# Kernel tuning notes

Measured on AMD Instinct MI355X. Metric: run time of the kernel, lower is better.

The kernel has to match this reference:

```python
import jax, jax.numpy as jnp
import numpy as np

N, M_X, M_G = 4096, 500, 50  # users, rating items, genre items


def setup_inputs() -> dict:
    key = jax.random.key(0)
    k1, k2, k3 = jax.random.split(key, 3)
    x_idx = jax.random.randint(k1, (N, M_X), 0, 6)          # ratings 0..5 (0 = pad)
    genre_idx = jax.random.randint(k2, (N, M_G), 0, 21)     # genre ids 0..20 (0 = pad)
    x1, x2, x3, x4, x5 = 3.0, 1.0, -1.0, -3.0, -5.0
    W_x = jnp.array([[0., 0., 0., 0., 0.],
                     [x1, x2, x3, x4, x5],
                     [x2, x1, x2, x3, x4],
                     [x3, x2, x1, x2, x3],
                     [x4, x3, x2, x1, x2],
                     [x5, x4, x3, x2, x1]], dtype=jnp.float32)  # [6,5]
    ohe_x = jnp.concatenate([jnp.zeros((1, 5)), jnp.eye(5)], axis=0).astype(jnp.float32)      # [6,5]
    W_genre = jax.random.normal(k3, (21, 20), dtype=jnp.float32)                              # [21,20]
    ohe_genre = jnp.concatenate([jnp.zeros((1, 20)), jnp.eye(20)], axis=0).astype(jnp.float32)  # [21,20]
    beta = jnp.array([1.0], dtype=jnp.float32)
    gamma = jnp.array([0.565], dtype=jnp.float32)
    coef = jnp.array([0.5, 0.001, 0.001], dtype=jnp.float32)
    return {"x_idx": x_idx, "genre_idx": genre_idx, "W_x": W_x, "ohe_x": ohe_x,
            "W_genre": W_genre, "ohe_genre": ohe_genre, "beta": beta, "gamma": gamma, "coef": coef}


def reference(x_idx, genre_idx, W_x, ohe_x, W_genre, ohe_genre, beta, gamma, coef):
    n = x_idx.shape[0]
    # Embeddings: table-lookup then flatten [N, items*dim]
    emb_x = W_x[x_idx].reshape(n, -1)        # [N, 2500]
    emb_xb = ohe_x[x_idx].reshape(n, -1)
    emb_g = W_genre[genre_idx].reshape(n, -1)  # [N, 1000]
    emb_gb = ohe_genre[genre_idx].reshape(n, -1)
    onehot = jnp.concatenate([emb_x, emb_g], axis=-1)       # [N, D]
    onehot_b = jnp.concatenate([emb_xb, emb_gb], axis=-1)   # [N, D]

    x = x_idx.astype(jnp.float32)            # [N, M]
    maskf = (x > 0).astype(jnp.float32)

    # Attention: one-hot similarity, diagonal mask, pow-temperature softmax
    sims = onehot @ onehot_b.T               # [N, N]
    sims = sims * (1.0 - jnp.eye(n, dtype=sims.dtype))
    temperature = jnp.power(jnp.max(sims, axis=1) + 0.001, gamma[0]) * beta[0]
    sim = jax.nn.softmax(sims / temperature[:, None], axis=1)

    mult = sim @ x                           # [N, M]
    scale = sim @ maskf + 0.0001             # [N, M]
    res = mult / scale

    # MeanAdd correction terms
    means_rows = x.sum(axis=1) / (maskf.sum(axis=1) + 1e-05)   # [N]
    means_cols = x.sum(axis=0) / (maskf.sum(axis=0) + 1e-05)   # [M]
    means_rows_m = maskf * means_rows[:, None]                 # [N, M]
    means_rows_sum = (sim @ means_rows_m) / scale
    means_rows_add = means_rows[:, None] - means_rows_sum
    add = (means_rows_add * coef[0]
           + (means_cols - means_cols.mean())[None, :] * coef[1]
           + (means_rows - means_rows.mean())[:, None] * coef[2])

    return jnp.clip(res + add, 1.0, 5.0)     # Hardtanh(1, 5)
```

## Files before the change

kernel.cpp:

```cpp
#include <hip/hip_runtime.h>
#include <hip/hip_bf16.h>
#include <stdint.h>

typedef unsigned short u16;
typedef unsigned int   u32;
typedef unsigned char  u8;
typedef long long      i64;
typedef __attribute__((ext_vector_type(8)))  __bf16 bf16x8;
typedef __attribute__((ext_vector_type(4)))  int    i32x4;
typedef __attribute__((ext_vector_type(16))) int    i32x16;
typedef __attribute__((ext_vector_type(16))) float  f32x16;

#define DEV __device__ __forceinline__

#define N_USERS 4096
#define MX      500
#define MG      50
#define K8      3584
#define RN      1536

#define OFF_A8  ((size_t)0)
#define OFF_B8  ((size_t)16777216)
#define OFF_P   ((size_t)0)
#define OFF_R   ((size_t)37748736)
#define OFF_S   ((size_t)58720256)
#define OFF_O   ((size_t)58720256)
#define OFF_SC  ((size_t)138412032)
#define OFF_WX8 (OFF_SC + 2048)
#define OFF_WG8 (OFF_SC + 2112)
#define OFF_MR  (OFF_SC + 4096)
#define OFF_MC  (OFF_SC + 4096 + 16384)
#define WS_REQUIRED (OFF_MC + 4096)

DEV u16 f2bf(float f) {
  union { float f; u32 u; } v; v.f = f;
  u32 r = v.u + 0x7FFFu + ((v.u >> 16) & 1u);
  return (u16)(r >> 16);
}
DEV float bf2f(u16 u) {
  union { u32 u; float f; } v; v.u = ((u32)u) << 16;
  return v.f;
}

DEV u8 f2fp8(float x) {
  union { float f; u32 u; } v; v.f = x;
  u32 s = (v.u >> 24) & 0x80u;
  float a = fabsf(x);
  if (a > 448.f) a = 448.f;
  if (a < 0.015625f) {
    int q = (int)rintf(a * 512.f);
    return (u8)(s | (u32)q);
  }
  v.f = a;
  int e = ((v.u >> 23) & 0xFF) - 127;
  u32 m = v.u & 0x7FFFFF;
  u32 mm = m >> 20;
  u32 rem = m & 0xFFFFF;
  if (rem > 0x80000u || (rem == 0x80000u && (mm & 1))) mm++;
  u32 out = (((u32)(e + 7)) << 3) + mm;
  if (out > 0x7Eu) out = 0x7Eu;
  return (u8)(s | out);
}

DEV void glds16(const void* g, void* l) {
  __builtin_amdgcn_global_load_lds(
      (const __attribute__((address_space(1))) void*)g,
      (__attribute__((address_space(3))) void*)l, 16, 0, 0);
}

__global__ __launch_bounds__(256) void k_prep(const void* wx, const void* wg,
                                              const void* beta, const void* gamma,
                                              const void* coef, float* sc,
                                              char* wx8, char* wg8) {
  __shared__ int sflag;
  int t = threadIdx.x;
  if (t == 0) {
    u32 u = ((const u32*)wx)[5];
    int f = (u == 0x40400000u) ? 1 : 0;
    sflag = f;
    ((int*)sc)[0] = f;
  }
  __syncthreads();
  int f = sflag;
  auto rd = [&](const void* p, int i) -> float {
    return f ? ((const float*)p)[i] : bf2f(((const u16*)p)[i]);
  };
  if (t == 0) {
    sc[1] = rd(beta, 0); sc[2] = rd(gamma, 0);
    sc[3] = rd(coef, 0); sc[4] = rd(coef, 1); sc[5] = rd(coef, 2);
  }
  for (int i = t; i < 30;  i += 256) wx8[i] = (char)__float2int_rn(rd(wx, i));
  for (int i = t; i < 420; i += 256) {
    int q = __float2int_rn(32.0f * rd(wg, i));
    q = (q > 127) ? 127 : ((q < -127) ? -127 : q);
    wg8[i] = (char)q;
  }
}

__global__ __launch_bounds__(64) void k_means_rows(const int* __restrict__ x, float* __restrict__ mr) {
  int i = blockIdx.x, t = threadIdx.x;
  const int* row = x + (size_t)i * MX;
  float s = 0.f, c = 0.f;
  for (int m = t; m < MX; m += 64) { int a = row[m]; s += (float)a; c += (a > 0) ? 1.f : 0.f; }
  for (int off = 32; off >= 1; off >>= 1) { s += __shfl_xor(s, off); c += __shfl_xor(c, off); }
  if (t == 0) mr[i] = s / (c + 1e-5f);
}

__global__ __launch_bounds__(256) void k_means_cols(const int* __restrict__ x, float* __restrict__ mc) {
  int m = blockIdx.x, t = threadIdx.x;
  float s = 0.f, c = 0.f;
  for (int i = t; i < N_USERS; i += 256) { int a = x[(size_t)i * MX + m]; s += (float)a; c += (a > 0) ? 1.f : 0.f; }
  __shared__ float ss[4], cs[4];
  for (int off = 32; off >= 1; off >>= 1) { s += __shfl_xor(s, off); c += __shfl_xor(c, off); }
  int w = t >> 6, lane = t & 63;
  if (lane == 0) { ss[w] = s; cs[w] = c; }
  __syncthreads();
  if (t == 0) {
    s = ss[0] + ss[1] + ss[2] + ss[3];
    c = cs[0] + cs[1] + cs[2] + cs[3];
    mc[m] = s / (c + 1e-5f);
  }
}

__global__ __launch_bounds__(256) void k_scalars(const float* __restrict__ mr, const float* __restrict__ mc, float* sc) {
  int t = threadIdx.x;
  float s1 = 0.f, s2 = 0.f;
  for (int i = t; i < N_USERS; i += 256) s1 += mr[i];
  for (int i = t; i < MX; i += 256) s2 += mc[i];
  __shared__ float a1[4], a2[4];
  for (int off = 32; off >= 1; off >>= 1) { s1 += __shfl_xor(s1, off); s2 += __shfl_xor(s2, off); }
  int w = t >> 6, lane = t & 63;
  if (lane == 0) { a1[w] = s1; a2[w] = s2; }
  __syncthreads();
  if (t == 0) {
    sc[6] = (a1[0] + a1[1] + a1[2] + a1[3]) / (float)N_USERS;
    sc[7] = (a2[0] + a2[1] + a2[2] + a2[3]) / (float)MX;
  }
}

__global__ __launch_bounds__(256) void k_buildAB(const int* __restrict__ xi, const int* __restrict__ gi,
                                                 const char* __restrict__ wx8, const char* __restrict__ wg8,
                                                 char* __restrict__ A8, char* __restrict__ B8) {
  int i = blockIdx.x, t = threadIdx.x;
  char* a8 = A8 + (size_t)i * K8;
  char* b8 = B8 + (size_t)i * K8;
  const int* xr = xi + (size_t)i * MX;
  const int* gr = gi + (size_t)i * MG;
  for (int m = t; m < MX; m += 256) {
    int a = xr[m];
    int base = m * 5;
#pragma unroll
    for (int d = 0; d < 5; ++d) {
      a8[base + d] = wx8[a * 5 + d];
      b8[base + d] = (a == d + 1) ? (char)32 : (char)0;
    }
  }
  for (int e = 2500 + t; e < 2560; e += 256) { a8[e] = 0; b8[e] = 0; }
  for (int m = t; m < MG; m += 256) {
    int g = gr[m];
    int base = 2560 + m * 20;
#pragma unroll
    for (int d = 0; d < 20; ++d) {
      a8[base + d] = wg8[g * 20 + d];
      b8[base + d] = (g == d + 1) ? (char)1 : (char)0;
    }
  }
  for (int e = 3560 + t; e < K8; e += 256) { a8[e] = 0; b8[e] = 0; }
}

__global__ __launch_bounds__(1024, 4) void k_gemm1(
    const char* __restrict__ A8, const char* __restrict__ B8,
    float* __restrict__ Cg, int N, int nt, int ld)
{
  extern __shared__ __align__(16) char ldsc[];
  int t = threadIdx.x, lane = t & 63, w = t >> 6;

  int nwg = gridDim.x * gridDim.y;
  int o = blockIdx.y * gridDim.x + blockIdx.x;
  int swz = (o & 7) * (nwg >> 3) + (o >> 3);
  int bn = swz % gridDim.x, bm = swz / gridDim.x;

  const char* pAb = A8 + (size_t)bm * 256 * ld;
  const char* pBb = B8 + (size_t)bn * 256 * ld;

  int wm = w >> 2, wn = w & 3;

  int aoffs[2][2], boffs[2][2];
#pragma unroll
  for (int m = 0; m < 2; ++m)
#pragma unroll
    for (int ks = 0; ks < 2; ++ks) {
      int row = wm * 64 + m * 32 + (lane & 31);
      int slot = ((ks << 1) | (lane >> 5)) ^ ((row & 3) ^ ((row >> 2) & 1));
      aoffs[m][ks] = row * 64 + slot * 16;
    }
#pragma unroll
  for (int n = 0; n < 2; ++n)
#pragma unroll
    for (int ks = 0; ks < 2; ++ks) {
      int col = wn * 64 + n * 32 + (lane & 31);
      int slot = ((ks << 1) | (lane >> 5)) ^ ((col & 3) ^ ((col >> 2) & 1));
      boffs[n][ks] = col * 64 + slot * 16;
    }

  const char* srcs[2]; int dsto[2];
  {
    const char* bp = (w < 8) ? pAb : pBb;
#pragma unroll
    for (int c = 0; c < 2; ++c) {
      int q = (w & 7) * 2 + c;
      int row = q * 16 + (lane >> 2);
      int slot = (lane & 3) ^ ((row & 3) ^ ((row >> 2) & 1));
      dsto[c] = ((w < 8) ? 0 : 16384) + q * 1024;
      srcs[c] = bp + (size_t)row * ld + slot * 16;
    }
  }

  auto stage = [&](int s) {
    if (s >= nt) return;
    char* dst = ldsc + ((size_t)(s & 3) << 15);
    size_t ko = (size_t)s * 64;
    glds16(srcs[0] + ko, dst + dsto[0]);
    glds16(srcs[1] + ko, dst + dsto[1]);
  };

#define STEP_TAIL(s)                                                        \
  do {                                                                      \
    int r_ = nt - 1 - (s);                                                  \
    if (r_ >= 3)      asm volatile("s_waitcnt vmcnt(4)" ::: "memory");      \
    else if (r_ == 2) asm volatile("s_waitcnt vmcnt(2)" ::: "memory");      \
    else if (r_ == 1) asm volatile("s_waitcnt vmcnt(0)" ::: "memory");      \
    if (r_ >= 1) {                                                          \
      __builtin_amdgcn_s_barrier();                                         \
      __builtin_amdgcn_sched_barrier(0);                                    \
    }                                                                       \
  } while (0)

  stage(0); stage(1); stage(2);
  asm volatile("s_waitcnt vmcnt(4)" ::: "memory");
  __builtin_amdgcn_s_barrier();
  __builtin_amdgcn_sched_barrier(0);

  i32x16 acc[2][2] = {};

  for (int s = 0; s < nt; ++s) {
    const char* At = ldsc + ((size_t)(s & 3) << 15);
    const char* Bt = At + 16384;
    stage(s + 3);
    i32x4 av[2][2], bv[2][2];
#pragma unroll
    for (int m = 0; m < 2; ++m)
#pragma unroll
      for (int ks = 0; ks < 2; ++ks) av[m][ks] = *(const i32x4*)(At + aoffs[m][ks]);
#pragma unroll
    for (int n = 0; n < 2; ++n)
#pragma unroll
      for (int ks = 0; ks < 2; ++ks) bv[n][ks] = *(const i32x4*)(Bt + boffs[n][ks]);
    __builtin_amdgcn_s_setprio(1);
#pragma unroll
    for (int ks = 0; ks < 2; ++ks)
#pragma unroll
      for (int m = 0; m < 2; ++m)
#pragma unroll
        for (int n = 0; n < 2; ++n)
          acc[m][n] = __builtin_amdgcn_mfma_i32_32x32x32_i8(av[m][ks], bv[n][ks], acc[m][n], 0, 0, 0);
    __builtin_amdgcn_s_setprio(0);
    STEP_TAIL(s);
  }
#undef STEP_TAIL

  int colb = bn * 256 + wn * 64 + (lane & 31);
  int rowb = bm * 256 + wm * 64 + ((lane >> 5) << 2);
#pragma unroll
  for (int m = 0; m < 2; ++m)
#pragma unroll
    for (int n = 0; n < 2; ++n) {
      float* Cp = Cg + (size_t)(rowb + m * 32) * N + colb + n * 32;
#pragma unroll
      for (int r = 0; r < 16; ++r) {
        int rr = (r & 3) + 8 * (r >> 2);
        Cp[(size_t)rr * N] = (float)acc[m][n][r] * 0.03125f;
      }
    }
}

__global__ __launch_bounds__(256, 2) void k_gemm2(
    const u8* __restrict__ Pg, const u8* __restrict__ Rg,
    float* __restrict__ Cg, int N, int nt, int ldp, int ldr)
{
  extern __shared__ __align__(16) char ldsc[];
  int t = threadIdx.x, lane = t & 63, w = t >> 6;

  int nwg = gridDim.x * gridDim.y;
  int o = blockIdx.y * gridDim.x + blockIdx.x;
  int swz = (o & 7) * (nwg >> 3) + (o >> 3);
  int bn = swz % gridDim.x, bm = swz / gridDim.x;

  const u8* pA = Pg + (size_t)bm * 128 * ldp;
  const u8* pB = Rg + (size_t)bn * 128 * ldr;

  int wm = w >> 1, wn = w & 1;

  int aoffs[2][4], boffs[2][4];
#pragma unroll
  for (int m = 0; m < 2; ++m)
#pragma unroll
    for (int kc = 0; kc < 4; ++kc) {
      int row = wm * 64 + m * 32 + (lane & 31);
      int slot = kc ^ ((row & 3) ^ ((row >> 2) & 1));
      aoffs[m][kc] = row * 64 + slot * 16 + ((lane >> 5) << 3);
    }
#pragma unroll
  for (int n = 0; n < 2; ++n)
#pragma unroll
    for (int kc = 0; kc < 4; ++kc) {
      int col = wn * 64 + n * 32 + (lane & 31);
      int slot = kc ^ ((col & 3) ^ ((col >> 2) & 1));
      boffs[n][kc] = 8192 + col * 64 + slot * 16 + ((lane >> 5) << 3);
    }

  const u8* srcs[4]; int dsto[4];
  {
    const u8* bsrc = (w < 2) ? pA : pB;
    int ld = (w < 2) ? ldp : ldr;
#pragma unroll
    for (int c = 0; c < 4; ++c) {
      int q = (w & 1) * 4 + c;
      int row = q * 16 + (lane >> 2);
      int slot = (lane & 3) ^ ((row & 3) ^ ((row >> 2) & 1));
      dsto[c] = ((w < 2) ? 0 : 8192) + q * 1024;
      srcs[c] = bsrc + (size_t)row * ld + slot * 16;
    }
  }

  auto stage = [&](int s) {
    if (s >= nt) return;
    char* dst = ldsc + ((size_t)(s & 3) << 14);
    size_t ko = (size_t)s * 64;
#pragma unroll
    for (int c = 0; c < 4; ++c) glds16(srcs[c] + ko, dst + dsto[c]);
  };

#define STEP_TAIL2(s)                                                       \
  do {                                                                      \
    int r_ = nt - 1 - (s);                                                  \
    if (r_ >= 3)      asm volatile("s_waitcnt vmcnt(8)" ::: "memory");      \
    else if (r_ == 2) asm volatile("s_waitcnt vmcnt(4)" ::: "memory");      \
    else if (r_ == 1) asm volatile("s_waitcnt vmcnt(0)" ::: "memory");      \
    if (r_ >= 1) {                                                          \
      __builtin_amdgcn_s_barrier();                                         \
      __builtin_amdgcn_sched_barrier(0);                                    \
    }                                                                       \
  } while (0)

  stage(0); stage(1); stage(2);
  asm volatile("s_waitcnt vmcnt(8)" ::: "memory");
  __builtin_amdgcn_s_barrier();
  __builtin_amdgcn_sched_barrier(0);

  f32x16 acc[2][2] = {};

  for (int s = 0; s < nt; ++s) {
    const char* At = ldsc + ((size_t)(s & 3) << 14);
    stage(s + 3);
    i64 av[2][4], bv[2][4];
#pragma unroll
    for (int m = 0; m < 2; ++m)
#pragma unroll
      for (int kc = 0; kc < 4; ++kc) av[m][kc] = *(const i64*)(At + aoffs[m][kc]);
#pragma unroll
    for (int n = 0; n < 2; ++n)
#pragma unroll
      for (int kc = 0; kc < 4; ++kc) bv[n][kc] = *(const i64*)(At + boffs[n][kc]);
    __builtin_amdgcn_s_setprio(1);
#pragma unroll
    for (int kc = 0; kc < 4; ++kc)
#pragma unroll
      for (int m = 0; m < 2; ++m)
#pragma unroll
        for (int n = 0; n < 2; ++n)
          acc[m][n] = __builtin_amdgcn_mfma_f32_32x32x16_fp8_fp8(av[m][kc], bv[n][kc], acc[m][n], 0, 0, 0);
    __builtin_amdgcn_s_setprio(0);
    STEP_TAIL2(s);
  }
#undef STEP_TAIL2

  int colb = bn * 128 + wn * 64 + (lane & 31);
  int rowb = bm * 128 + wm * 64 + ((lane >> 5) << 2);
#pragma unroll
  for (int m = 0; m < 2; ++m)
#pragma unroll
    for (int n = 0; n < 2; ++n) {
      float* Cp = Cg + (size_t)(rowb + m * 32) * N + colb + n * 32;
#pragma unroll
      for (int r = 0; r < 16; ++r) {
        int rr = (r & 3) + 8 * (r >> 2);
        Cp[(size_t)rr * N] = acc[m][n][r] * 0.00390625f;
      }
    }
}

__global__ __launch_bounds__(256) void k_softmax(const float* __restrict__ S, u8* __restrict__ P,
                                                 const float* __restrict__ sc) {
  int i = blockIdx.x, t = threadIdx.x;
  const float* row = S + (size_t)i * N_USERS;
  float v[16];
#pragma unroll
  for (int c = 0; c < 4; ++c) {
    float4 f = *(const float4*)&row[(c * 256 + t) * 4];
    v[c * 4 + 0] = f.x; v[c * 4 + 1] = f.y; v[c * 4 + 2] = f.z; v[c * 4 + 3] = f.w;
  }
#pragma unroll
  for (int c = 0; c < 4; ++c) {
    int j0 = (c * 256 + t) * 4;
#pragma unroll
    for (int q = 0; q < 4; ++q) if (j0 + q == i) v[c * 4 + q] = 0.f;
  }
  float mx = -1e30f;
#pragma unroll
  for (int e = 0; e < 16; ++e) mx = fmaxf(mx, v[e]);
  __shared__ float red[8];
  for (int off = 32; off >= 1; off >>= 1) mx = fmaxf(mx, __shfl_xor(mx, off));
  int w = t >> 6, lane = t & 63;
  if (lane == 0) red[w] = mx;
  __syncthreads();
  mx = fmaxf(fmaxf(red[0], red[1]), fmaxf(red[2], red[3]));

  float invT = 1.f / (powf(mx + 0.001f, sc[2]) * sc[1]);
  float s = 0.f;
#pragma unroll
  for (int e = 0; e < 16; ++e) { v[e] = expf((v[e] - mx) * invT); s += v[e]; }
  for (int off = 32; off >= 1; off >>= 1) s += __shfl_xor(s, off);
  if (lane == 0) red[4 + w] = s;
  __syncthreads();
  s = red[4] + red[5] + red[6] + red[7];
  float rs = 256.f / s;

  u8* prow = P + (size_t)i * N_USERS;
#pragma unroll
  for (int c = 0; c < 4; ++c) {
    int j0 = (c * 256 + t) * 4;
    u32 pk = 0;
#pragma unroll
    for (int q = 0; q < 4; ++q) pk |= ((u32)f2fp8(v[c * 4 + q] * rs)) << (q * 8);
    *(u32*)&prow[j0] = pk;
  }
}

__global__ __launch_bounds__(256) void k_buildRt(const int* __restrict__ xi, const float* __restrict__ mr,
                                                 const float* __restrict__ sc, u8* __restrict__ R) {
  __shared__ u8 tile[64][68];
  int k0 = blockIdx.x * 64;
  int n0 = blockIdx.y * 64;
  int t = threadIdx.x;
  int c = t & 63, r0 = t >> 6;
  float cm = sc[6];

  int n = n0 + c;
#pragma unroll
  for (int i = 0; i < 16; ++i) {
    int r = r0 + i * 4;
    int k = k0 + r;
    u8 v = 0;
    if (n < 500) {
      int a = xi[(size_t)k * MX + n];
      v = f2fp8((float)a);
    } else if (n < 1000) {
      int a = xi[(size_t)k * MX + (n - 500)];
      v = (a > 0) ? (u8)0x38 : (u8)0;
    } else if (n < 1500) {
      int a = xi[(size_t)k * MX + (n - 1000)];
      v = (a > 0) ? f2fp8(mr[k] - cm) : (u8)0;
    }
    tile[r][c] = v;
  }
  __syncthreads();

  int kw = t & 15, cb = t >> 4;
#pragma unroll
  for (int i = 0; i < 4; ++i) {
    int cc = cb + i * 16;
    u32 wv = (u32)tile[kw * 4 + 0][cc]
           | ((u32)tile[kw * 4 + 1][cc] << 8)
           | ((u32)tile[kw * 4 + 2][cc] << 16)
           | ((u32)tile[kw * 4 + 3][cc] << 24);
    *(u32*)&R[(size_t)(n0 + cc) * N_USERS + k0 + kw * 4] = wv;
  }
}

__global__ __launch_bounds__(256) void k_final(const float* __restrict__ O, const float* __restrict__ mr,
                                               const float* __restrict__ mc, const float* __restrict__ sc,
                                               void* __restrict__ out) {
  int m = blockIdx.x * 256 + threadIdx.x;
  int i = blockIdx.y;
  if (m >= MX) return;
  const float* o0 = O + (size_t)i * RN;
  float mult  = o0[m];
  float o2    = o0[500 + m];
  float o3    = o0[1000 + m];
  float c0 = sc[3], c1 = sc[4], c2 = sc[5], mrm = sc[6], mcm = sc[7];
  float scale = o2 + 1e-4f;
  float res   = mult / scale;
  float mrs   = (o3 + mrm * o2) / scale;
  float add = (mr[i] - mrs) * c0 + (mc[m] - mcm) * c1 + (mr[i] - mrm) * c2;
  float r = res + add;
  r = fminf(fmaxf(r, 1.f), 5.f);
  int f32mode = ((const int*)sc)[0];
  if (f32mode) ((float*)out)[(size_t)i * MX + m] = r;
  else         ((u16*)out)[(size_t)i * MX + m] = f2bf(r);
}

extern "C" void kernel_launch(void* const* d_in, const int* in_sizes, int n_in,
                              void* d_out, int out_size, void* d_ws, size_t ws_size,
                              hipStream_t stream) {
  if (ws_size < WS_REQUIRED) return;
  const int* xi = (const int*)d_in[0];
  const int* gi = (const int*)d_in[1];
  char* ws = (char*)d_ws;
  char*  A8  = ws + OFF_A8;
  char*  B8  = ws + OFF_B8;
  u8*    P   = (u8*)(ws + OFF_P);
  float* S   = (float*)(ws + OFF_S);
  float* O   = (float*)(ws + OFF_O);
  u8*    R   = (u8*)(ws + OFF_R);
  float* sc  = (float*)(ws + OFF_SC);
  char*  wx8 = ws + OFF_WX8;
  char*  wg8 = ws + OFF_WG8;
  float* mr  = (float*)(ws + OFF_MR);
  float* mc  = (float*)(ws + OFF_MC);

  (void)hipFuncSetAttribute((const void*)k_gemm1,
                            hipFuncAttributeMaxDynamicSharedMemorySize, 131072);
  (void)hipFuncSetAttribute((const void*)k_gemm2,
                            hipFuncAttributeMaxDynamicSharedMemorySize, 65536);

  k_prep<<<1, 256, 0, stream>>>(d_in[2], d_in[4], d_in[6], d_in[7], d_in[8], sc, wx8, wg8);
  k_means_rows<<<N_USERS, 64, 0, stream>>>(xi, mr);
  k_means_cols<<<MX, 256, 0, stream>>>(xi, mc);
  k_scalars<<<1, 256, 0, stream>>>(mr, mc, sc);
  k_buildAB<<<N_USERS, 256, 0, stream>>>(xi, gi, wx8, wg8, A8, B8);
  k_gemm1<<<dim3(16, 16, 1), 1024, 131072, stream>>>(A8, B8, S, N_USERS, K8 / 64, K8);
  k_softmax<<<N_USERS, 256, 0, stream>>>(S, P, sc);
  k_buildRt<<<dim3(64, 24), 256, 0, stream>>>(xi, mr, sc, R);
  k_gemm2<<<dim3(RN / 128, 32), 256, 65536, stream>>>(
      P, R, O, RN, N_USERS / 64, N_USERS, N_USERS);
  k_final<<<dim3(2, N_USERS), 256, 0, stream>>>(O, mr, mc, sc, d_out);
}
```

Measured before the change: 200.3 us.

## Fuse final epilogue into second GEMM and row means into buildAB

The second GEMM is restructured so that each block loads the matching columns of the three R segments (mult, mask and mean-row terms), each padded to 512. The MeanAdd/clip epilogue is computed directly in registers, which removes the O intermediate buffer and the k_final kernel. Row means are now computed inside k_buildAB, which removes the k_means_rows launch. The trade-off is a larger LDS stage (20 KB per stage), a 2x3 accumulator tile with more registers, and some wasted columns in the padded segments.

```diff
diff --git a/kernel.cpp b/kernel.cpp
--- a/kernel.cpp
+++ b/kernel.cpp
@@ -24,7 +24,6 @@
 #define OFF_P   ((size_t)0)
 #define OFF_R   ((size_t)37748736)
 #define OFF_S   ((size_t)58720256)
-#define OFF_O   ((size_t)58720256)
 #define OFF_SC  ((size_t)138412032)
 #define OFF_WX8 (OFF_SC + 2048)
 #define OFF_WG8 (OFF_SC + 2112)
@@ -97,15 +96,6 @@
   }
 }
 
-__global__ __launch_bounds__(64) void k_means_rows(const int* __restrict__ x, float* __restrict__ mr) {
-  int i = blockIdx.x, t = threadIdx.x;
-  const int* row = x + (size_t)i * MX;
-  float s = 0.f, c = 0.f;
-  for (int m = t; m < MX; m += 64) { int a = row[m]; s += (float)a; c += (a > 0) ? 1.f : 0.f; }
-  for (int off = 32; off >= 1; off >>= 1) { s += __shfl_xor(s, off); c += __shfl_xor(c, off); }
-  if (t == 0) mr[i] = s / (c + 1e-5f);
-}
-
 __global__ __launch_bounds__(256) void k_means_cols(const int* __restrict__ x, float* __restrict__ mc) {
   int m = blockIdx.x, t = threadIdx.x;
   float s = 0.f, c = 0.f;
@@ -140,14 +130,17 @@
 
 __global__ __launch_bounds__(256) void k_buildAB(const int* __restrict__ xi, const int* __restrict__ gi,
                                                  const char* __restrict__ wx8, const char* __restrict__ wg8,
-                                                 char* __restrict__ A8, char* __restrict__ B8) {
+                                                 char* __restrict__ A8, char* __restrict__ B8,
+                                                 float* __restrict__ mr) {
   int i = blockIdx.x, t = threadIdx.x;
   char* a8 = A8 + (size_t)i * K8;
   char* b8 = B8 + (size_t)i * K8;
   const int* xr = xi + (size_t)i * MX;
   const int* gr = gi + (size_t)i * MG;
+  float s = 0.f, c = 0.f;
   for (int m = t; m < MX; m += 256) {
     int a = xr[m];
+    s += (float)a; c += (a > 0) ? 1.f : 0.f;
     int base = m * 5;
 #pragma unroll
     for (int d = 0; d < 5; ++d) {
@@ -166,6 +159,16 @@
     }
   }
   for (int e = 3560 + t; e < K8; e += 256) { a8[e] = 0; b8[e] = 0; }
+  __shared__ float rs[4], rc[4];
+  for (int off = 32; off >= 1; off >>= 1) { s += __shfl_xor(s, off); c += __shfl_xor(c, off); }
+  int w = t >> 6, lane = t & 63;
+  if (lane == 0) { rs[w] = s; rc[w] = c; }
+  __syncthreads();
+  if (t == 0) {
+    s = rs[0] + rs[1] + rs[2] + rs[3];
+    c = rc[0] + rc[1] + rc[2] + rc[3];
+    mr[i] = s / (c + 1e-5f);
+  }
 }
 
 __global__ __launch_bounds__(1024, 4) void k_gemm1(
@@ -284,9 +287,10 @@
     }
 }
 
-__global__ __launch_bounds__(256, 2) void k_gemm2(
+__global__ __launch_bounds__(256, 2) void k_gemm2f(
     const u8* __restrict__ Pg, const u8* __restrict__ Rg,
-    float* __restrict__ Cg, int N, int nt, int ldp, int ldr)
+    const float* __restrict__ mr, const float* __restrict__ mc,
+    const float* __restrict__ sc, void* __restrict__ out, int nt)
 {
   extern __shared__ __align__(16) char ldsc[];
   int t = threadIdx.x, lane = t & 63, w = t >> 6;
@@ -294,14 +298,12 @@
   int nwg = gridDim.x * gridDim.y;
   int o = blockIdx.y * gridDim.x + blockIdx.x;
   int swz = (o & 7) * (nwg >> 3) + (o >> 3);
-  int bn = swz % gridDim.x, bm = swz / gridDim.x;
-
-  const u8* pA = Pg + (size_t)bm * 128 * ldp;
-  const u8* pB = Rg + (size_t)bn * 128 * ldr;
-
+  int bx = swz % gridDim.x, by = swz / gridDim.x;
+
+  const u8* pA = Pg + (size_t)by * 128 * N_USERS;
   int wm = w >> 1, wn = w & 1;
 
-  int aoffs[2][4], boffs[2][4];
+  int aoffs[2][4];
 #pragma unroll
   for (int m = 0; m < 2; ++m)
 #pragma unroll
@@ -310,43 +312,48 @@
       int slot = kc ^ ((row & 3) ^ ((row >> 2) & 1));
       aoffs[m][kc] = row * 64 + slot * 16 + ((lane >> 5) << 3);
     }
-#pragma unroll
-  for (int n = 0; n < 2; ++n)
+  int boffs[3][4];
+#pragma unroll
+  for (int sg = 0; sg < 3; ++sg)
 #pragma unroll
     for (int kc = 0; kc < 4; ++kc) {
-      int col = wn * 64 + n * 32 + (lane & 31);
-      int slot = kc ^ ((col & 3) ^ ((col >> 2) & 1));
-      boffs[n][kc] = 8192 + col * 64 + slot * 16 + ((lane >> 5) << 3);
-    }
-
-  const u8* srcs[4]; int dsto[4];
-  {
-    const u8* bsrc = (w < 2) ? pA : pB;
-    int ld = (w < 2) ? ldp : ldr;
-#pragma unroll
-    for (int c = 0; c < 4; ++c) {
-      int q = (w & 1) * 4 + c;
-      int row = q * 16 + (lane >> 2);
+      int br = sg * 64 + wn * 32 + (lane & 31);
+      int slot = kc ^ ((br & 3) ^ ((br >> 2) & 1));
+      boffs[sg][kc] = 8192 + br * 64 + slot * 16 + ((lane >> 5) << 3);
+    }
+
+  const u8* srcs[5]; int dsto[5];
+#pragma unroll
+  for (int c5 = 0; c5 < 5; ++c5) {
+    int call = w * 5 + c5;
+    if (call < 8) {
+      int row = call * 16 + (lane >> 2);
       int slot = (lane & 3) ^ ((row & 3) ^ ((row >> 2) & 1));
-      dsto[c] = ((w < 2) ? 0 : 8192) + q * 1024;
-      srcs[c] = bsrc + (size_t)row * ld + slot * 16;
+      dsto[c5] = call * 1024;
+      srcs[c5] = pA + (size_t)row * N_USERS + slot * 16;
+    } else {
+      int brow = (call - 8) * 16 + (lane >> 2);
+      int sg = brow >> 6, within = brow & 63;
+      int slot = (lane & 3) ^ ((brow & 3) ^ ((brow >> 2) & 1));
+      dsto[c5] = 8192 + (call - 8) * 1024;
+      srcs[c5] = Rg + (size_t)(sg * 512 + bx * 64 + within) * N_USERS + slot * 16;
     }
   }
 
   auto stage = [&](int s) {
     if (s >= nt) return;
-    char* dst = ldsc + ((size_t)(s & 3) << 14);
+    char* dst = ldsc + (size_t)(s & 3) * 20480;
     size_t ko = (size_t)s * 64;
 #pragma unroll
-    for (int c = 0; c < 4; ++c) glds16(srcs[c] + ko, dst + dsto[c]);
+    for (int c5 = 0; c5 < 5; ++c5) glds16(srcs[c5] + ko, dst + dsto[c5]);
   };
 
 #define STEP_TAIL2(s)                                                       \
   do {                                                                      \
     int r_ = nt - 1 - (s);                                                  \
-    if (r_ >= 3)      asm volatile("s_waitcnt vmcnt(8)" ::: "memory");      \
-    else if (r_ == 2) asm volatile("s_waitcnt vmcnt(4)" ::: "memory");      \
-    else if (r_ == 1) asm volatile("s_waitcnt vmcnt(0)" ::: "memory");      \
+    if (r_ >= 3)      asm volatile("s_waitcnt vmcnt(10)" ::: "memory");     \
+    else if (r_ == 2) asm volatile("s_waitcnt vmcnt(5)"  ::: "memory");     \
+    else if (r_ == 1) asm volatile("s_waitcnt vmcnt(0)"  ::: "memory");     \
     if (r_ >= 1) {                                                          \
       __builtin_amdgcn_s_barrier();                                         \
       __builtin_amdgcn_sched_barrier(0);                                    \
@@ -354,50 +361,62 @@
   } while (0)
 
   stage(0); stage(1); stage(2);
-  asm volatile("s_waitcnt vmcnt(8)" ::: "memory");
+  asm volatile("s_waitcnt vmcnt(10)" ::: "memory");
   __builtin_amdgcn_s_barrier();
   __builtin_amdgcn_sched_barrier(0);
 
-  f32x16 acc[2][2] = {};
+  f32x16 acc[2][3] = {};
 
   for (int s = 0; s < nt; ++s) {
-    const char* At = ldsc + ((size_t)(s & 3) << 14);
+    const char* At = ldsc + (size_t)(s & 3) * 20480;
     stage(s + 3);
-    i64 av[2][4], bv[2][4];
+    i64 av[2][4], bv[3][4];
 #pragma unroll
     for (int m = 0; m < 2; ++m)
 #pragma unroll
       for (int kc = 0; kc < 4; ++kc) av[m][kc] = *(const i64*)(At + aoffs[m][kc]);
 #pragma unroll
-    for (int n = 0; n < 2; ++n)
-#pragma unroll
-      for (int kc = 0; kc < 4; ++kc) bv[n][kc] = *(const i64*)(At + boffs[n][kc]);
+    for (int sg = 0; sg < 3; ++sg)
+#pragma unroll
+      for (int kc = 0; kc < 4; ++kc) bv[sg][kc] = *(const i64*)(At + boffs[sg][kc]);
     __builtin_amdgcn_s_setprio(1);
 #pragma unroll
     for (int kc = 0; kc < 4; ++kc)
 #pragma unroll
       for (int m = 0; m < 2; ++m)
 #pragma unroll
-        for (int n = 0; n < 2; ++n)
-          acc[m][n] = __builtin_amdgcn_mfma_f32_32x32x16_fp8_fp8(av[m][kc], bv[n][kc], acc[m][n], 0, 0, 0);
+        for (int sg = 0; sg < 3; ++sg)
+          acc[m][sg] = __builtin_amdgcn_mfma_f32_32x32x16_fp8_fp8(av[m][kc], bv[sg][kc], acc[m][sg], 0, 0, 0);
     __builtin_amdgcn_s_setprio(0);
     STEP_TAIL2(s);
   }
 #undef STEP_TAIL2
 
-  int colb = bn * 128 + wn * 64 + (lane & 31);
-  int rowb = bm * 128 + wm * 64 + ((lane >> 5) << 2);
-#pragma unroll
-  for (int m = 0; m < 2; ++m)
-#pragma unroll
-    for (int n = 0; n < 2; ++n) {
-      float* Cp = Cg + (size_t)(rowb + m * 32) * N + colb + n * 32;
-#pragma unroll
-      for (int r = 0; r < 16; ++r) {
-        int rr = (r & 3) + 8 * (r >> 2);
-        Cp[(size_t)rr * N] = acc[m][n][r] * 0.00390625f;
+  float c0 = sc[3], c1 = sc[4], c2 = sc[5], mrm = sc[6], mcm = sc[7];
+  int f32mode = ((const int*)sc)[0];
+  int mcol = bx * 64 + wn * 32 + (lane & 31);
+  float mcv = (mcol < 500) ? mc[mcol] : 0.f;
+  int rowb = by * 128 + wm * 64 + ((lane >> 5) << 2);
+#pragma unroll
+  for (int m = 0; m < 2; ++m) {
+#pragma unroll
+    for (int r = 0; r < 16; ++r) {
+      int i = rowb + m * 32 + (r & 3) + 8 * (r >> 2);
+      float o1 = acc[m][0][r] * 0.00390625f;
+      float o2 = acc[m][1][r] * 0.00390625f;
+      float o3 = acc[m][2][r] * 0.00390625f;
+      float scale = o2 + 1e-4f;
+      float res = o1 / scale;
+      float mrs = (o3 + mrm * o2) / scale;
+      float mri = mr[i];
+      float add = (mri - mrs) * c0 + (mcv - mcm) * c1 + (mri - mrm) * c2;
+      float rr = fminf(fmaxf(res + add, 1.f), 5.f);
+      if (mcol < 500) {
+        if (f32mode) ((float*)out)[(size_t)i * MX + mcol] = rr;
+        else         ((u16*)out)[(size_t)i * MX + mcol] = f2bf(rr);
       }
     }
+  }
 }
 
 __global__ __launch_bounds__(256) void k_softmax(const float* __restrict__ S, u8* __restrict__ P,
@@ -457,20 +476,17 @@
   float cm = sc[6];
 
   int n = n0 + c;
+  int seg = n >> 9, m = n & 511;
 #pragma unroll
   for (int i = 0; i < 16; ++i) {
     int r = r0 + i * 4;
     int k = k0 + r;
     u8 v = 0;
-    if (n < 500) {
-      int a = xi[(size_t)k * MX + n];
-      v = f2fp8((float)a);
-    } else if (n < 1000) {
-      int a = xi[(size_t)k * MX + (n - 500)];
-      v = (a > 0) ? (u8)0x38 : (u8)0;
-    } else if (n < 1500) {
-      int a = xi[(size_t)k * MX + (n - 1000)];
-      v = (a > 0) ? f2fp8(mr[k] - cm) : (u8)0;
+    if (m < 500) {
+      int a = xi[(size_t)k * MX + m];
+      if (seg == 0)      v = f2fp8((float)a);
+      else if (seg == 1) v = (a > 0) ? (u8)0x38 : (u8)0;
+      else               v = (a > 0) ? f2fp8(mr[k] - cm) : (u8)0;
     }
     tile[r][c] = v;
   }
@@ -486,28 +502,6 @@
            | ((u32)tile[kw * 4 + 3][cc] << 24);
     *(u32*)&R[(size_t)(n0 + cc) * N_USERS + k0 + kw * 4] = wv;
   }
-}
-
-__global__ __launch_bounds__(256) void k_final(const float* __restrict__ O, const float* __restrict__ mr,
-                                               const float* __restrict__ mc, const float* __restrict__ sc,
-                                               void* __restrict__ out) {
-  int m = blockIdx.x * 256 + threadIdx.x;
-  int i = blockIdx.y;
-  if (m >= MX) return;
-  const float* o0 = O + (size_t)i * RN;
-  float mult  = o0[m];
-  float o2    = o0[500 + m];
-  float o3    = o0[1000 + m];
-  float c0 = sc[3], c1 = sc[4], c2 = sc[5], mrm = sc[6], mcm = sc[7];
-  float scale = o2 + 1e-4f;
-  float res   = mult / scale;
-  float mrs   = (o3 + mrm * o2) / scale;
-  float add = (mr[i] - mrs) * c0 + (mc[m] - mcm) * c1 + (mr[i] - mrm) * c2;
-  float r = res + add;
-  r = fminf(fmaxf(r, 1.f), 5.f);
-  int f32mode = ((const int*)sc)[0];
-  if (f32mode) ((float*)out)[(size_t)i * MX + m] = r;
-  else         ((u16*)out)[(size_t)i * MX + m] = f2bf(r);
 }
 
 extern "C" void kernel_launch(void* const* d_in, const int* in_sizes, int n_in,
@@ -521,7 +515,6 @@
   char*  B8  = ws + OFF_B8;
   u8*    P   = (u8*)(ws + OFF_P);
   float* S   = (float*)(ws + OFF_S);
-  float* O   = (float*)(ws + OFF_O);
   u8*    R   = (u8*)(ws + OFF_R);
   float* sc  = (float*)(ws + OFF_SC);
   char*  wx8 = ws + OFF_WX8;
@@ -531,18 +524,15 @@
 
   (void)hipFuncSetAttribute((const void*)k_gemm1,
                             hipFuncAttributeMaxDynamicSharedMemorySize, 131072);
-  (void)hipFuncSetAttribute((const void*)k_gemm2,
-                            hipFuncAttributeMaxDynamicSharedMemorySize, 65536);
+  (void)hipFuncSetAttribute((const void*)k_gemm2f,
+                            hipFuncAttributeMaxDynamicSharedMemorySize, 81920);
 
   k_prep<<<1, 256, 0, stream>>>(d_in[2], d_in[4], d_in[6], d_in[7], d_in[8], sc, wx8, wg8);
-  k_means_rows<<<N_USERS, 64, 0, stream>>>(xi, mr);
+  k_buildAB<<<N_USERS, 256, 0, stream>>>(xi, gi, wx8, wg8, A8, B8, mr);
   k_means_cols<<<MX, 256, 0, stream>>>(xi, mc);
   k_scalars<<<1, 256, 0, stream>>>(mr, mc, sc);
-  k_buildAB<<<N_USERS, 256, 0, stream>>>(xi, gi, wx8, wg8, A8, B8);
   k_gemm1<<<dim3(16, 16, 1), 1024, 131072, stream>>>(A8, B8, S, N_USERS, K8 / 64, K8);
   k_softmax<<<N_USERS, 256, 0, stream>>>(S, P, sc);
   k_buildRt<<<dim3(64, 24), 256, 0, stream>>>(xi, mr, sc, R);
-  k_gemm2<<<dim3(RN / 128, 32), 256, 65536, stream>>>(
-      P, R, O, RN, N_USERS / 64, N_USERS, N_USERS);
-  k_final<<<dim3(2, N_USERS), 256, 0, stream>>>(O, mr, mc, sc, d_out);
-}
+  k_gemm2f<<<dim3(8, 32), 256, 81920, stream>>>(P, R, mr, mc, sc, d_out, N_USERS / 64);
+}
```

New measurement: 191.8 us. -4.2%, faster.
